# Performance work log

Hardware: AMD Instinct MI355X
Metric: run time of the kernel (lower is better)

Reference implementation:

```python
import jax, jax.numpy as jnp
import numpy as np

FOCAL_GAMMA = 2.0
DIRECTIONAL_PENALTY = 1.5
CONFIDENCE_WEIGHT = 0.1
PENALTY_MATRIX = jnp.array([[0.0, 0.5, 1.5],
                            [0.5, 0.0, 0.5],
                            [1.5, 0.5, 0.0]], dtype=jnp.float32)

BATCH = 8388608
NUM_CLASSES = 3


def setup_inputs() -> dict:
    key = jax.random.key(0)
    k1, k2, k3 = jax.random.split(key, 3)
    logits = jax.random.normal(k1, (BATCH, NUM_CLASSES), dtype=jnp.float32)
    targets = jax.random.randint(k2, (BATCH,), 0, NUM_CLASSES, dtype=jnp.int32)
    class_weights = jax.random.uniform(k3, (NUM_CLASSES,), dtype=jnp.float32) + 0.5
    return {"logits": logits, "targets": targets, "class_weights": class_weights}


def reference(logits, targets, class_weights):
    # softmax probs and argmax predictions
    log_probs = jax.nn.log_softmax(logits, axis=-1)            # [B, 3]
    probs = jnp.exp(log_probs)
    predictions = jnp.argmax(logits, axis=-1)                  # [B]

    # focal loss (alpha applied after unweighted CE, as in the torch code)
    ce = -jnp.take_along_axis(log_probs, targets[:, None], axis=-1)[:, 0]  # [B]
    p_t = jnp.exp(-ce)
    focal_weight = (1.0 - p_t) ** FOCAL_GAMMA
    alpha_t = class_weights[targets]
    base_loss = jnp.mean(alpha_t * focal_weight * ce)

    # directional penalty: vectorized gather over penalty matrix
    penalties = PENALTY_MATRIX[predictions, targets]            # [B]
    directional_loss = jnp.mean(penalties) * DIRECTIONAL_PENALTY

    # confidence calibration: penalize confident wrong predictions
    correct = (predictions == targets).astype(probs.dtype)
    max_probs = jnp.max(probs, axis=-1)
    confidence_loss = CONFIDENCE_WEIGHT * jnp.mean((1.0 - correct) * max_probs)

    return base_loss + directional_loss + confidence_loss
```

## Files before the change

### kernel.cpp

```cpp
#include <hip/hip_runtime.h>

#define FOCAL_GAMMA_IS_2 1
#define DIRECTIONAL_PENALTY 1.5f
#define CONFIDENCE_WEIGHT 0.1f

__global__ __launch_bounds__(256) void trading_loss_kernel(
    const float* __restrict__ logits,
    const int*   __restrict__ targets,
    const float* __restrict__ cw,
    float*       __restrict__ out,
    int nquads,
    float inv_b)
{
    const float w0 = cw[0], w1 = cw[1], w2 = cw[2];

    const float4* __restrict__ lg4 = (const float4*)logits;
    const int4*   __restrict__ tg4 = (const int4*)targets;

    float acc = 0.0f;
    int tid    = blockIdx.x * blockDim.x + threadIdx.x;
    int stride = gridDim.x * blockDim.x;

    for (int q = tid; q < nquads; q += stride) {
        float4 v0 = lg4[3 * q + 0];
        float4 v1 = lg4[3 * q + 1];
        float4 v2 = lg4[3 * q + 2];
        int4   tg = tg4[q];

        float ra[4] = {v0.x, v0.w, v1.z, v2.y};
        float rb[4] = {v0.y, v1.x, v1.w, v2.z};
        float rc[4] = {v0.z, v1.y, v2.x, v2.w};
        int   tt[4] = {tg.x, tg.y, tg.z, tg.w};

        #pragma unroll
        for (int r = 0; r < 4; ++r) {
            float a = ra[r], b = rb[r], c = rc[r];
            int t = tt[r];

            int pred = 0;
            float m = a;
            if (b > m) { m = b; pred = 1; }
            if (c > m) { m = c; pred = 2; }

            float e0 = __expf(a - m);
            float e1 = __expf(b - m);
            float e2 = __expf(c - m);
            float s = e0 + e1 + e2;
            float inv_s = 1.0f / s;

            float et = (t == 0) ? e0 : ((t == 1) ? e1 : e2);
            float lt = (t == 0) ? a  : ((t == 1) ? b  : c);
            float p_t = et * inv_s;
            float ce = (m - lt) + __logf(s);

            float w  = (t == 0) ? w0 : ((t == 1) ? w1 : w2);
            float omp = 1.0f - p_t;
            float contrib = w * omp * omp * ce;

            int d = pred - t; d = (d < 0) ? -d : d;
            float pen = (d == 1) ? 0.5f : ((d == 2) ? 1.5f : 0.0f);
            contrib += DIRECTIONAL_PENALTY * pen;

            if (pred != t) contrib += CONFIDENCE_WEIGHT * inv_s;

            acc += contrib;
        }
    }

    #pragma unroll
    for (int off = 32; off > 0; off >>= 1)
        acc += __shfl_down(acc, off, 64);

    __shared__ float sdata[4];
    int lane = threadIdx.x & 63;
    int wid  = threadIdx.x >> 6;
    if (lane == 0) sdata[wid] = acc;
    __syncthreads();
    if (threadIdx.x == 0) {
        float bsum = sdata[0] + sdata[1] + sdata[2] + sdata[3];
        atomicAdd(out, bsum * inv_b);
    }
}

extern "C" void kernel_launch(void* const* d_in, const int* in_sizes, int n_in,
                              void* d_out, int out_size, void* d_ws, size_t ws_size,
                              hipStream_t stream) {
    const float* logits  = (const float*)d_in[0];
    const int*   targets = (const int*)d_in[1];
    const float* cw      = (const float*)d_in[2];
    float* out = (float*)d_out;

    const int B = in_sizes[1];
    const int nquads = B / 4;
    const float inv_b = 1.0f / (float)B;

    hipMemsetAsync(out, 0, out_size * sizeof(float), stream);

    const int threads = 256;
    const int blocks  = 2048;
    trading_loss_kernel<<<blocks, threads, 0, stream>>>(
        logits, targets, cw, out, nquads, inv_b);
}
```

Measured before the change: 180.2 us.

## Stage logits through shared memory and replace atomics with two-pass reduction

```diff
diff --git a/kernel.cpp b/kernel.cpp
--- a/kernel.cpp
+++ b/kernel.cpp
@@ -1,70 +1,78 @@
 #include <hip/hip_runtime.h>
 
-#define FOCAL_GAMMA_IS_2 1
 #define DIRECTIONAL_PENALTY 1.5f
 #define CONFIDENCE_WEIGHT 0.1f
 
-__global__ __launch_bounds__(256) void trading_loss_kernel(
+__device__ __forceinline__ float row_loss(float a, float b, float c, int t,
+                                          float w0, float w1, float w2) {
+    int pred = 0;
+    float m = a;
+    if (b > m) { m = b; pred = 1; }
+    if (c > m) { m = c; pred = 2; }
+
+    float e0 = __expf(a - m);
+    float e1 = __expf(b - m);
+    float e2 = __expf(c - m);
+    float s = e0 + e1 + e2;
+    float inv_s = 1.0f / s;
+
+    float et = (t == 0) ? e0 : ((t == 1) ? e1 : e2);
+    float lt = (t == 0) ? a  : ((t == 1) ? b  : c);
+    float p_t = et * inv_s;
+    float ce = (m - lt) + __logf(s);
+
+    float w  = (t == 0) ? w0 : ((t == 1) ? w1 : w2);
+    float omp = 1.0f - p_t;
+    float contrib = w * omp * omp * ce;
+
+    int d = pred - t; d = (d < 0) ? -d : d;
+    float pen = (d == 1) ? 0.5f : ((d == 2) ? 1.5f : 0.0f);
+    contrib += DIRECTIONAL_PENALTY * pen;
+
+    if (pred != t) contrib += CONFIDENCE_WEIGHT * inv_s;
+    return contrib;
+}
+
+__global__ __launch_bounds__(256) void tsl_partial(
     const float* __restrict__ logits,
     const int*   __restrict__ targets,
     const float* __restrict__ cw,
-    float*       __restrict__ out,
-    int nquads,
-    float inv_b)
+    float*       __restrict__ partial,
+    int nTiles, int B)
 {
+    __shared__ __align__(16) float smem[3072];
     const float w0 = cw[0], w1 = cw[1], w2 = cw[2];
-
-    const float4* __restrict__ lg4 = (const float4*)logits;
-    const int4*   __restrict__ tg4 = (const int4*)targets;
+    const int tid = threadIdx.x;
 
     float acc = 0.0f;
-    int tid    = blockIdx.x * blockDim.x + threadIdx.x;
-    int stride = gridDim.x * blockDim.x;
 
-    for (int q = tid; q < nquads; q += stride) {
-        float4 v0 = lg4[3 * q + 0];
-        float4 v1 = lg4[3 * q + 1];
-        float4 v2 = lg4[3 * q + 2];
-        int4   tg = tg4[q];
+    for (int tile = blockIdx.x; tile < nTiles; tile += gridDim.x) {
+        const float4* __restrict__ g4 = (const float4*)logits + (size_t)tile * 768;
+        float4* s4 = (float4*)smem;
+        s4[tid]       = g4[tid];
+        s4[tid + 256] = g4[tid + 256];
+        s4[tid + 512] = g4[tid + 512];
+        __syncthreads();
 
-        float ra[4] = {v0.x, v0.w, v1.z, v2.y};
-        float rb[4] = {v0.y, v1.x, v1.w, v2.z};
-        float rc[4] = {v0.z, v1.y, v2.x, v2.w};
-        int   tt[4] = {tg.x, tg.y, tg.z, tg.w};
+        const int rowBase = tile * 1024;
+        #pragma unroll
+        for (int j = 0; j < 4; ++j) {
+            const int lr = tid + 256 * j;
+            float a = smem[3 * lr + 0];
+            float b = smem[3 * lr + 1];
+            float c = smem[3 * lr + 2];
+            int   t = targets[rowBase + lr];
+            acc += row_loss(a, b, c, t, w0, w1, w2);
+        }
+        __syncthreads();
+    }
 
-        #pragma unroll
-        for (int r = 0; r < 4; ++r) {
-            float a = ra[r], b = rb[r], c = rc[r];
-            int t = tt[r];
-
-            int pred = 0;
-            float m = a;
-            if (b > m) { m = b; pred = 1; }
-            if (c > m) { m = c; pred = 2; }
-
-            float e0 = __expf(a - m);
-            float e1 = __expf(b - m);
-            float e2 = __expf(c - m);
-            float s = e0 + e1 + e2;
-            float inv_s = 1.0f / s;
-
-            float et = (t == 0) ? e0 : ((t == 1) ? e1 : e2);
-            float lt = (t == 0) ? a  : ((t == 1) ? b  : c);
-            float p_t = et * inv_s;
-            float ce = (m - lt) + __logf(s);
-
-            float w  = (t == 0) ? w0 : ((t == 1) ? w1 : w2);
-            float omp = 1.0f - p_t;
-            float contrib = w * omp * omp * ce;
-
-            int d = pred - t; d = (d < 0) ? -d : d;
-            float pen = (d == 1) ? 0.5f : ((d == 2) ? 1.5f : 0.0f);
-            contrib += DIRECTIONAL_PENALTY * pen;
-
-            if (pred != t) contrib += CONFIDENCE_WEIGHT * inv_s;
-
-            acc += contrib;
-        }
+    for (int r = nTiles * 1024 + blockIdx.x * 256 + tid; r < B;
+         r += gridDim.x * 256) {
+        float a = logits[3 * r + 0];
+        float b = logits[3 * r + 1];
+        float c = logits[3 * r + 2];
+        acc += row_loss(a, b, c, targets[r], w0, w1, w2);
     }
 
     #pragma unroll
@@ -72,14 +80,32 @@
         acc += __shfl_down(acc, off, 64);
 
     __shared__ float sdata[4];
-    int lane = threadIdx.x & 63;
-    int wid  = threadIdx.x >> 6;
+    const int lane = tid & 63;
+    const int wid  = tid >> 6;
     if (lane == 0) sdata[wid] = acc;
     __syncthreads();
-    if (threadIdx.x == 0) {
-        float bsum = sdata[0] + sdata[1] + sdata[2] + sdata[3];
-        atomicAdd(out, bsum * inv_b);
-    }
+    if (tid == 0)
+        partial[blockIdx.x] = sdata[0] + sdata[1] + sdata[2] + sdata[3];
+}
+
+__global__ __launch_bounds__(256) void tsl_final(
+    const float* __restrict__ partial, int n,
+    float* __restrict__ out, float inv_b)
+{
+    float acc = 0.0f;
+    for (int i = threadIdx.x; i < n; i += 256) acc += partial[i];
+
+    #pragma unroll
+    for (int off = 32; off > 0; off >>= 1)
+        acc += __shfl_down(acc, off, 64);
+
+    __shared__ float sdata[4];
+    const int lane = threadIdx.x & 63;
+    const int wid  = threadIdx.x >> 6;
+    if (lane == 0) sdata[wid] = acc;
+    __syncthreads();
+    if (threadIdx.x == 0)
+        out[0] = (sdata[0] + sdata[1] + sdata[2] + sdata[3]) * inv_b;
 }
 
 extern "C" void kernel_launch(void* const* d_in, const int* in_sizes, int n_in,
@@ -88,16 +114,14 @@
     const float* logits  = (const float*)d_in[0];
     const int*   targets = (const int*)d_in[1];
     const float* cw      = (const float*)d_in[2];
-    float* out = (float*)d_out;
+    float* out     = (float*)d_out;
+    float* partial = (float*)d_ws;
 
     const int B = in_sizes[1];
-    const int nquads = B / 4;
+    const int nTiles = B / 1024;
     const float inv_b = 1.0f / (float)B;
 
-    hipMemsetAsync(out, 0, out_size * sizeof(float), stream);
-
-    const int threads = 256;
-    const int blocks  = 2048;
-    trading_loss_kernel<<<blocks, threads, 0, stream>>>(
-        logits, targets, cw, out, nquads, inv_b);
+    const int blocks = 2048;
+    tsl_partial<<<blocks, 256, 0, stream>>>(logits, targets, cw, partial, nTiles, B);
+    tsl_final<<<1, 256, 0, stream>>>(partial, blocks, out, inv_b);
 }
```

After: 176.3 us. 2.2% less time.
